# Kernel tuning notes

Hardware: AMD Instinct MI355X
Metric: run time of the kernel (lower is better)

The kernel has to match this reference:

```python
import jax, jax.numpy as jnp
import numpy as np
from jax.scipy.linalg import solve_triangular

B, M, S, NBPS = 32768, 16, 8, 4
NUM_ITER = 2
EPS = 1e-4

def _pam_gray(b):
    if len(b) > 1:
        return (1 - 2 * b[0]) * (2 ** len(b[1:]) - _pam_gray(b[1:]))
    return 1 - 2 * b[0]

def _qam(nbps):
    n = 2 ** nbps
    pts = np.zeros(n, np.complex64)
    for i in range(n):
        b = np.array([int(c) for c in np.binary_repr(i, nbps)])
        pts[i] = _pam_gray(b[0::2]) + 1j * _pam_gray(b[1::2])
    pts = pts / np.sqrt(np.mean(np.abs(pts) ** 2))
    labels = ((np.arange(n)[:, None] >> np.arange(nbps - 1, -1, -1)) & 1).astype(np.float32)
    return pts.astype(np.complex64), labels

_PTS_NP, _LAB_NP = _qam(NBPS)
PTS = jnp.asarray(_PTS_NP)                                   # [P] complex64, unit-energy Gray QAM16
PTS_E = jnp.asarray((np.abs(_PTS_NP) ** 2).astype(np.float32))  # [P]
LAB = jnp.asarray(_LAB_NP)                                   # [P, K] bit labels (MSB first)
ASGN = 2.0 * LAB - 1.0                                       # [P, K], +1 where bit==1

def _symbol_logits(llr):
    # LLRs2SymbolLogits: llr=[...,S,K] (llr = log p(b=1)/p(b=0)) -> per-point log-prior [...,S,P]
    return jnp.sum(jax.nn.log_sigmoid(ASGN * llr[..., None, :]), axis=-1)

def _moments(logits):
    # SymbolLogits2Moments: softmax over points -> mean / variance of soft symbols
    p = jax.nn.softmax(logits, axis=-1)                       # [..., S, P]
    mean = jnp.einsum('...p,p->...', p.astype(jnp.complex64), PTS)
    e2 = jnp.einsum('...p,p->...', p, PTS_E)
    var = e2 - (mean.real ** 2 + mean.imag ** 2)
    return mean, var

def _demap(x_hat, llr_a, no_eff):
    # maxlog DemapperWithPrior, LLR = log p(b=1)/p(b=0)
    diff = x_hat[..., None] - PTS                             # [..., S, P]
    d2 = diff.real ** 2 + diff.imag ** 2
    exps = -d2 / no_eff[..., None] + _symbol_logits(llr_a)    # [..., S, P]
    e = exps[..., None]                                       # [..., S, P, 1]
    neg = jnp.float32(-1e30)
    l1 = jnp.max(jnp.where(LAB == 1.0, e, neg), axis=-2)      # [..., S, K]
    l0 = jnp.max(jnp.where(LAB == 0.0, e, neg), axis=-2)
    return l1 - l0

def _forward(y_re, y_im, h_re, h_im, prior, s_re, s_im):
    y = jax.lax.complex(y_re, y_im)                           # [B, M]
    h = jax.lax.complex(h_re, h_im)                           # [B, M, S]
    s = jax.lax.complex(s_re, s_im)                           # [B, M, M] Hermitian PSD
    # whiten_channel: s = L L^H, y <- L^-1 y, h <- L^-1 h
    L = jnp.linalg.cholesky(s)
    y = solve_triangular(L, y[..., None], lower=True)[..., 0]
    h = solve_triangular(L, h, lower=True)
    y_mf = jnp.einsum('bms,bm->bs', jnp.conj(h), y)[..., None]   # [B, S, 1] matched filter
    g = jnp.einsum('bmi,bmj->bij', jnp.conj(h), h)               # [B, S, S] Gram matrix
    # real-valued channel representation [[Re,-Im],[Im,Re]]
    hr = jnp.concatenate([
        jnp.concatenate([h.real, -h.imag], axis=-1),
        jnp.concatenate([h.imag, h.real], axis=-1)], axis=-2)    # [B, 2M, 2S]
    gr = jnp.einsum('bmi,bmj->bij', hr, hr)                      # [B, 2S, 2S]
    eye2s = jnp.eye(2 * S, dtype=jnp.float32)
    llr_d = prior
    llr_a = jnp.zeros_like(prior)
    for _ in range(NUM_ITER):
        llr_a = llr_d
        x_hat, var_x = _moments(_symbol_logits(llr_a))           # [B, S]
        # parallel interference cancellation in matched-filter domain
        y_mf_pic = (y_mf + g * x_hat[..., None, :]
                    - jnp.einsum('bij,bj->bi', g, x_hat)[..., None])  # [B, S, S]
        var2 = jnp.concatenate([var_x, var_x], axis=-1)          # [B, 2S]
        a = gr * var2[..., None, :] + eye2s                      # [B, 2S, 2S]
        a_inv = jnp.linalg.inv(a)
        mu = jnp.sum(a_inv * jnp.swapaxes(gr, -1, -2), axis=-1)  # diag(a_inv @ gr), [B, 2S]
        ypt = jnp.swapaxes(y_mf_pic, -1, -2)                     # [B, S, S] (stream-major)
        ypt_r = jnp.concatenate([ypt.real, ypt.imag], axis=-1)   # [B, S, 2S]
        ypt_r = jnp.concatenate([ypt_r, ypt_r], axis=-2)         # [B, 2S, 2S]
        z = jnp.sum(a_inv * ypt_r, axis=-1) / mu                 # [B, 2S] unbiased estimates
        zr, zi = jnp.split(z, 2, axis=-1)
        x_hat = jax.lax.complex(zr, zi)                          # [B, S]
        rho = mu / jnp.maximum(1.0 - var2 * mu, EPS)             # post-equalization SINR
        rho = jnp.split(rho, 2, axis=-1)[0]                      # [B, S]
        no_eff = 1.0 / rho
        llr_d = _demap(x_hat, llr_a, no_eff)
    return llr_d - llr_a  # extrinsic LLRs [B, S, K]

def setup_inputs() -> dict:
    key = jax.random.key(0)
    k = jax.random.split(key, 7)
    y_re = jax.random.normal(k[0], (B, M), jnp.float32)
    y_im = jax.random.normal(k[1], (B, M), jnp.float32)
    h_re = jax.random.normal(k[2], (B, M, S), jnp.float32) / np.float32(np.sqrt(2.0))
    h_im = jax.random.normal(k[3], (B, M, S), jnp.float32) / np.float32(np.sqrt(2.0))
    prior = 0.5 * jax.random.normal(k[4], (B, S, NBPS), jnp.float32)
    a = jax.lax.complex(jax.random.normal(k[5], (B, M, M), jnp.float32),
                        jax.random.normal(k[6], (B, M, M), jnp.float32)) / np.float32(np.sqrt(2.0 * M))
    s = jnp.einsum('bij,bkj->bik', a, jnp.conj(a)) + 0.5 * jnp.eye(M, dtype=jnp.complex64)
    return {"y_re": y_re, "y_im": y_im, "h_re": h_re, "h_im": h_im,
            "prior": prior, "s_re": s.real, "s_im": s.imag}

def reference(y_re, y_im, h_re, h_im, prior, s_re, s_im):
    return _forward(y_re, y_im, h_re, h_im, prior, s_re, s_im)
```

## Files before the change

kernel.cpp:

```cpp
#include <hip/hip_runtime.h>


#define EPS_F 1e-4f
#define INV_SQRT10 0.31622776601683794f
#define WSYNC() __builtin_amdgcn_wave_barrier()

__device__ __forceinline__ float rcpf(float x) { return __builtin_amdgcn_rcpf(x); }
__device__ __forceinline__ float rsqf(float x) { return __builtin_amdgcn_rsqf(x); }
__device__ __forceinline__ float rdlane(float v, int l) {
    return __uint_as_float(__builtin_amdgcn_readlane(__float_as_uint(v), l));
}
template<int OFF>
__device__ __forceinline__ float swzf(float v) {
    return __uint_as_float(__builtin_amdgcn_ds_swizzle(__float_as_uint(v), OFF));
}
#define SWX1 0x041F
#define SWX2 0x081F
#define SWX4 0x101F

__device__ __forceinline__ float pt_re(int p) {
    return (1.0f - 2.0f * (float)((p >> 3) & 1)) * (1.0f + 2.0f * (float)((p >> 1) & 1)) * INV_SQRT10;
}
__device__ __forceinline__ float pt_im(int p) {
    return (1.0f - 2.0f * (float)((p >> 2) & 1)) * (1.0f + 2.0f * (float)(p & 1)) * INV_SQRT10;
}

__global__ __launch_bounds__(128, 4)
void mmse_pic_kernel(const float* __restrict__ y_re, const float* __restrict__ y_im,
                     const float* __restrict__ h_re, const float* __restrict__ h_im,
                     const float* __restrict__ prior,
                     const float* __restrict__ s_re, const float* __restrict__ s_im,
                     float* __restrict__ out)
{
    const int lane = threadIdx.x & 63;
    const int w    = threadIdx.x >> 6;
    const int b    = blockIdx.x * 2 + w;
    const size_t bs = (size_t)b;

    __shared__ float2 Sc[2][16][28];
    __shared__ float2 xc_[2][8];
    __shared__ float2 ymc_[2][8];
    __shared__ float  vx_[2][8], ne_[2][8];
    __shared__ float  lsig[2][64];
    __shared__ float  logit_[2][8][20];
    __shared__ float  llrD_[2][8][4];

    {
        const float4* pr4 = (const float4*)(s_re + bs * 256);
        const float4* pi4 = (const float4*)(s_im + bs * 256);
        float4 vr = pr4[lane], vi = pi4[lane];
        int r = lane >> 2, c0 = (lane & 3) << 2;
        Sc[w][r][c0+0] = make_float2(vr.x, vi.x);
        Sc[w][r][c0+1] = make_float2(vr.y, vi.y);
        Sc[w][r][c0+2] = make_float2(vr.z, vi.z);
        Sc[w][r][c0+3] = make_float2(vr.w, vi.w);
        if (lane < 32) {
            const float4* hr4 = (const float4*)(h_re + bs * 128);
            const float4* hi4 = (const float4*)(h_im + bs * 128);
            float4 hr = hr4[lane], hi = hi4[lane];
            int row = lane >> 1, col = 16 + ((lane & 1) << 2);
            Sc[w][row][col+0] = make_float2(hr.x, hi.x);
            Sc[w][row][col+1] = make_float2(hr.y, hi.y);
            Sc[w][row][col+2] = make_float2(hr.z, hi.z);
            Sc[w][row][col+3] = make_float2(hr.w, hi.w);
        }
        if (lane < 16) Sc[w][lane][24] = make_float2(y_re[bs*16+lane], y_im[bs*16+lane]);
        if (lane < 32) ((float*)llrD_[w])[lane] = prior[bs*32 + lane];
    }
    WSYNC();

    {
        const int j0 = lane & 15;
        const int r4 = lane >> 4;
        #pragma unroll
        for (int k = 0; k < 15; ++k) {
            float invd = rcpf(Sc[w][k][k].x);
            int j1 = k + 1 + j0, j2 = j1 + 16;
            float2 rk0 = make_float2(0.f, 0.f), rk1 = make_float2(0.f, 0.f);
            if (j1 < 25) rk0 = Sc[w][k][j1];
            const bool blk2 = (k < 8);
            if (blk2 && j2 < 25) rk1 = Sc[w][k][j2];
            const int pmin = (k + 1) >> 2;
            #pragma unroll
            for (int p = 0; p < 4; ++p) {
                if (p < pmin) continue;
                int i = (p << 2) + r4;
                float2 aik = Sc[w][i][k];
                float mr = aik.x * invd, mi = aik.y * invd;
                if (i <= k) { mr = 0.f; mi = 0.f; }
                if (j1 < 25) {
                    float2 a = Sc[w][i][j1];
                    a.x -= mr*rk0.x - mi*rk0.y;
                    a.y -= mr*rk0.y + mi*rk0.x;
                    Sc[w][i][j1] = a;
                }
                if (blk2 && j2 < 25) {
                    float2 a = Sc[w][i][j2];
                    a.x -= mr*rk1.x - mi*rk1.y;
                    a.y -= mr*rk1.y + mi*rk1.x;
                    Sc[w][i][j2] = a;
                }
            }
            WSYNC();
        }
    }
    {
        int r2 = lane >> 2, c = lane & 3;
        float irs = rsqf(Sc[w][r2][r2].x);
        float2 v0 = Sc[w][r2][16 + c];
        Sc[w][r2][16 + c] = make_float2(v0.x*irs, v0.y*irs);
        float2 v1 = Sc[w][r2][20 + c];
        Sc[w][r2][20 + c] = make_float2(v1.x*irs, v1.y*irs);
        if (c == 0) {
            float2 v2 = Sc[w][r2][24];
            Sc[w][r2][24] = make_float2(v2.x*irs, v2.y*irs);
        }
    }
    WSYNC();

    const int s = lane >> 3, u = lane & 7;
    float g_re = 0.f, g_im = 0.f, ym_r = 0.f, ym_i = 0.f;
    #pragma unroll
    for (int m = 0; m < 16; ++m) {
        float2 a  = Sc[w][m][16 + s];
        float2 x  = Sc[w][m][16 + u];
        float2 xy = Sc[w][m][24];
        g_re += a.x*x.x + a.y*x.y;
        g_im += a.x*x.y - a.y*x.x;
        ym_r += a.x*xy.x + a.y*xy.y;
        ym_i += a.x*xy.y - a.y*xy.x;
    }
    if (u == 0) ymc_[w][s] = make_float2(ym_r, ym_i);
    WSYNC();

    const float pr = pt_re(u), pi2 = pt_im(u), pe = pr*pr + pi2*pi2;
    float llr_a_reg = 0.f;

    for (int it = 0; it < 2; ++it) {
        {
            int ts = lane >> 3, tk = (lane >> 1) & 3, sg = lane & 1;
            float v = llrD_[w][ts][tk];
            float x = sg ? v : -v;
            lsig[w][lane] = fminf(x, 0.f) - __logf(1.0f + __expf(-fabsf(x)));
        }
        if (lane < 32) llr_a_reg = ((float*)llrD_[w])[lane];
        WSYNC();
        int base = s << 3;
        float lc = lsig[w][base | 2 | ((u >> 2) & 1)]
                 + lsig[w][base | 4 | ((u >> 1) & 1)]
                 + lsig[w][base | 6 | (u & 1)];
        float l0 = lc + lsig[w][base];
        float l1 = lc + lsig[w][base | 1];
        {
            float mx = fmaxf(l0, l1);
            mx = fmaxf(mx, swzf<SWX1>(mx));
            mx = fmaxf(mx, swzf<SWX2>(mx));
            mx = fmaxf(mx, swzf<SWX4>(mx));
            float w0 = __expf(l0 - mx), w1 = __expf(l1 - mx);
            float a = w0 + w1, dw = w0 - w1;
            float se = a, mr = dw * pr, mi = a * pi2, e2 = a * pe;
            se += swzf<SWX1>(se); mr += swzf<SWX1>(mr); mi += swzf<SWX1>(mi); e2 += swzf<SWX1>(e2);
            se += swzf<SWX2>(se); mr += swzf<SWX2>(mr); mi += swzf<SWX2>(mi); e2 += swzf<SWX2>(e2);
            se += swzf<SWX4>(se); mr += swzf<SWX4>(mr); mi += swzf<SWX4>(mi); e2 += swzf<SWX4>(e2);
            if (u == 0) {
                float inv = rcpf(se);
                float mxr = mr*inv, mxi = mi*inv;
                xc_[w][s] = make_float2(mxr, mxi);
                vx_[w][s] = e2*inv - (mxr*mxr + mxi*mxi);
            }
        }
        WSYNC();
        float2 xj = xc_[w][u];
        float vj = vx_[w][u];
        float tr = g_re*xj.x - g_im*xj.y;
        float ti = g_re*xj.y + g_im*xj.x;
        tr += swzf<SWX1>(tr); ti += swzf<SWX1>(ti);
        tr += swzf<SWX2>(tr); ti += swzf<SWX2>(ti);
        tr += swzf<SWX4>(tr); ti += swzf<SWX4>(ti);
        float2 ym = ymc_[w][s];
        float br_ = ym.x - tr, bi_ = ym.y - ti;
        float Ar = g_re*vj + ((s == u) ? 1.f : 0.f);
        float Ai = g_im*vj;
        float Cr = g_re, Ci = g_im;
        #define GJ_STEP(K) { \
            float pvr = rdlane(Ar, (K)*9), pvi = rdlane(Ai, (K)*9); \
            int rowsrc = ((K)<<3)|u; \
            float rAr = __shfl(Ar, rowsrc), rAi = __shfl(Ai, rowsrc); \
            float rCr = __shfl(Cr, rowsrc), rCi = __shfl(Ci, rowsrc); \
            float rbr = __shfl(br_, rowsrc), rbi = __shfl(bi_, rowsrc); \
            float cAr = swzf<(((K)<<5)|0x18)>(Ar), cAi = swzf<(((K)<<5)|0x18)>(Ai); \
            float id2 = rcpf(pvr*pvr + pvi*pvi); \
            float ipr2 = pvr*id2, ipi2 = -pvi*id2; \
            float mr2 = cAr*ipr2 - cAi*ipi2; \
            float mi2 = cAr*ipi2 + cAi*ipr2; \
            if (s == (K)) { mr2 = 0.f; mi2 = 0.f; } \
            Ar  -= mr2*rAr - mi2*rAi;  Ai  -= mr2*rAi + mi2*rAr; \
            Cr  -= mr2*rCr - mi2*rCi;  Ci  -= mr2*rCi + mi2*rCr; \
            br_ -= mr2*rbr - mi2*rbi;  bi_ -= mr2*rbi + mi2*rbr; }
        GJ_STEP(0) GJ_STEP(1) GJ_STEP(2) GJ_STEP(3)
        GJ_STEP(4) GJ_STEP(5) GJ_STEP(6) GJ_STEP(7)
        #undef GJ_STEP
        if (s == u) {
            float id3 = rcpf(Ar*Ar + Ai*Ai);
            float ipr3 = Ar*id3, ipi3 = -Ai*id3;
            float wr = br_*ipr3 - bi_*ipi3;
            float wi = br_*ipi3 + bi_*ipr3;
            float ccr = Cr*ipr3 - Ci*ipi3;
            float cci = Cr*ipi3 + Ci*ipr3;
            float mu = ccr;
            float im = rcpf(mu);
            float zr = (wr + ccr*xj.x - cci*xj.y) * im;
            float zi = (wi + ccr*xj.y + cci*xj.x) * im;
            xc_[w][s] = make_float2(zr, zi);
            ne_[w][s] = fmaxf(1.f - vx_[w][s]*mu, EPS_F) * im;
        }
        WSYNC();
        {
            float2 xh = xc_[w][s];
            float idn = rcpf(ne_[w][s]);
            float dr0 = xh.x - pr, dr1 = xh.x + pr, di = xh.y - pi2;
            logit_[w][s][u]     = l0 - (dr0*dr0 + di*di) * idn;
            logit_[w][s][u + 8] = l1 - (dr1*dr1 + di*di) * idn;
        }
        WSYNC();
        {
            int s2 = lane >> 3, kb = (lane >> 1) & 3, half = lane & 1;
            int bitpos = 3 - kb;
            float m = -1e30f;
            #pragma unroll
            for (int q = 0; q < 8; ++q) {
                int low  = q & ((1 << bitpos) - 1);
                int high = (q >> bitpos) << (bitpos + 1);
                int p = high | (half << bitpos) | low;
                m = fmaxf(m, logit_[w][s2][p]);
            }
            float other = swzf<SWX1>(m);
            if (half == 1) llrD_[w][s2][kb] = m - other;
        }
        WSYNC();
    }

    if (lane < 32) out[bs*32 + lane] = ((float*)llrD_[w])[lane] - llr_a_reg;
}

extern "C" void kernel_launch(void* const* d_in, const int* in_sizes, int n_in,
                              void* d_out, int out_size, void* d_ws, size_t ws_size,
                              hipStream_t stream) {
    const float* y_re  = (const float*)d_in[0];
    const float* y_im  = (const float*)d_in[1];
    const float* h_re  = (const float*)d_in[2];
    const float* h_im  = (const float*)d_in[3];
    const float* prior = (const float*)d_in[4];
    const float* s_re  = (const float*)d_in[5];
    const float* s_im  = (const float*)d_in[6];
    float* out = (float*)d_out;

    const int B = in_sizes[0] / 16;
    mmse_pic_kernel<<<dim3(B / 2), dim3(128), 0, stream>>>(
        y_re, y_im, h_re, h_im, prior, s_re, s_im, out);
}
```

Baseline: 232.4 us.

## Keep Gaussian elimination in registers using cross-lane swizzle and bpermute

The augmented 16x25 complex matrix now stays in per-lane registers during the forward elimination, with each lane holding 7 columns of one row. Pivot rows are broadcast with ds_swizzle and multipliers with ds_bpermute and readlane, replacing the LDS reads and writes and the wave barriers between pivot steps. Only the scaled H and y columns are written back to LDS. This cuts LDS traffic and synchronization, but every lane now processes all 7 register columns at every step, and it adds cross-lane instructions and register pressure.

```diff
diff --git a/kernel.cpp b/kernel.cpp
--- a/kernel.cpp
+++ b/kernel.cpp
@@ -13,6 +13,9 @@
 template<int OFF>
 __device__ __forceinline__ float swzf(float v) {
     return __uint_as_float(__builtin_amdgcn_ds_swizzle(__float_as_uint(v), OFF));
+}
+__device__ __forceinline__ float bpermf(int byteidx, float v) {
+    return __uint_as_float(__builtin_amdgcn_ds_bpermute(byteidx, __float_as_uint(v)));
 }
 #define SWX1 0x041F
 #define SWX2 0x081F
@@ -69,52 +72,48 @@
     }
     WSYNC();
 
+    const int rr = lane & 15, qq = lane >> 4;
+    float2 cc[7];
     {
-        const int j0 = lane & 15;
-        const int r4 = lane >> 4;
         #pragma unroll
-        for (int k = 0; k < 15; ++k) {
-            float invd = rcpf(Sc[w][k][k].x);
-            int j1 = k + 1 + j0, j2 = j1 + 16;
-            float2 rk0 = make_float2(0.f, 0.f), rk1 = make_float2(0.f, 0.f);
-            if (j1 < 25) rk0 = Sc[w][k][j1];
-            const bool blk2 = (k < 8);
-            if (blk2 && j2 < 25) rk1 = Sc[w][k][j2];
-            const int pmin = (k + 1) >> 2;
-            #pragma unroll
-            for (int p = 0; p < 4; ++p) {
-                if (p < pmin) continue;
-                int i = (p << 2) + r4;
-                float2 aik = Sc[w][i][k];
-                float mr = aik.x * invd, mi = aik.y * invd;
-                if (i <= k) { mr = 0.f; mi = 0.f; }
-                if (j1 < 25) {
-                    float2 a = Sc[w][i][j1];
-                    a.x -= mr*rk0.x - mi*rk0.y;
-                    a.y -= mr*rk0.y + mi*rk0.x;
-                    Sc[w][i][j1] = a;
-                }
-                if (blk2 && j2 < 25) {
-                    float2 a = Sc[w][i][j2];
-                    a.x -= mr*rk1.x - mi*rk1.y;
-                    a.y -= mr*rk1.y + mi*rk1.x;
-                    Sc[w][i][j2] = a;
-                }
-            }
-            WSYNC();
-        }
-    }
+        for (int j = 0; j < 7; ++j) cc[j] = Sc[w][rr][qq * 7 + j];
+    }
+    float irs = 0.f;
+    const int idxr4 = rr << 2;
+
+#define ELIM(K) { \
+        constexpr int GK = (K) / 7, SK = (K) % 7; \
+        const float dk = rdlane(cc[SK].x, GK * 16 + (K)); \
+        const float invd = rcpf(dk); \
+        if (rr == (K)) irs = rsqf(dk); \
+        const float akr = bpermf(idxr4 + GK * 64, cc[SK].x); \
+        const float aki = bpermf(idxr4 + GK * 64, cc[SK].y); \
+        float mr = akr * invd, mi = aki * invd; \
+        if (rr <= (K)) { mr = 0.f; mi = 0.f; } \
+        _Pragma("unroll") \
+        for (int j = 0; j < 7; ++j) { \
+            float pvr = swzf<(((K) << 5) | 0x10)>(cc[j].x); \
+            float pvi = swzf<(((K) << 5) | 0x10)>(cc[j].y); \
+            cc[j].x -= mr * pvr - mi * pvi; \
+            cc[j].y -= mr * pvi + mi * pvr; \
+        } }
+
+    ELIM(0)  ELIM(1)  ELIM(2)  ELIM(3)  ELIM(4)  ELIM(5)  ELIM(6)
+    ELIM(7)  ELIM(8)  ELIM(9)  ELIM(10) ELIM(11) ELIM(12) ELIM(13) ELIM(14)
+#undef ELIM
     {
-        int r2 = lane >> 2, c = lane & 3;
-        float irs = rsqf(Sc[w][r2][r2].x);
-        float2 v0 = Sc[w][r2][16 + c];
-        Sc[w][r2][16 + c] = make_float2(v0.x*irs, v0.y*irs);
-        float2 v1 = Sc[w][r2][20 + c];
-        Sc[w][r2][20 + c] = make_float2(v1.x*irs, v1.y*irs);
-        if (c == 0) {
-            float2 v2 = Sc[w][r2][24];
-            Sc[w][r2][24] = make_float2(v2.x*irs, v2.y*irs);
-        }
+        const float d15 = rdlane(cc[1].x, 47);
+        if (rr == 15) irs = rsqf(d15);
+    }
+
+    if (qq == 2) {
+        #pragma unroll
+        for (int j = 2; j < 7; ++j)
+            Sc[w][rr][14 + j] = make_float2(cc[j].x * irs, cc[j].y * irs);
+    } else if (qq == 3) {
+        #pragma unroll
+        for (int j = 0; j < 4; ++j)
+            Sc[w][rr][21 + j] = make_float2(cc[j].x * irs, cc[j].y * irs);
     }
     WSYNC();
 
```

Result: slower. 241.3 us (+3.8%).
